# Optimization experiments

Measured on AMD Instinct MI355X. Metric: run time of the kernel, lower is better.

## Reference

```python
import jax, jax.numpy as jnp
import numpy as np

B, N, D = 8, 256, 3          # batch, particles, spatial dims
H = 64                        # hidden_nf (channels)
L = 4                         # num_layers
ENC = 3                       # atom_type, aa_type, aa_pos
IN_NF = ENC + 1               # + time
COORDS_RANGE = 15.0 / L       # tanh=True -> coords_range/n_layers
E = B * N * N                 # fully-connected edges per batch graph


def _linear(key, fin, fout):
    k1, k2 = jax.random.split(key)
    s = 1.0 / np.sqrt(fin)
    w = jax.random.uniform(k1, (fout, fin), minval=-s, maxval=s, dtype=jnp.float32)
    b = jax.random.uniform(k2, (fout,), minval=-s, maxval=s, dtype=jnp.float32)
    return w, b


def setup_inputs() -> dict:
    key = jax.random.key(0)
    ks = jax.random.split(key, 64)
    inp = {
        "t": jax.random.uniform(ks[0], (B, 1), dtype=jnp.float32),
        "x": jax.random.normal(ks[1], (B, N * D), dtype=jnp.float32),
        "atom_type": jax.random.uniform(ks[2], (B, N), dtype=jnp.float32),
        "aa_type": jax.random.uniform(ks[3], (B, N), dtype=jnp.float32),
        "aa_pos": jax.random.uniform(ks[4], (B, N), dtype=jnp.float32),
        "node_mask": jnp.ones((B, N), dtype=jnp.float32),
    }
    inp["emb_w"], inp["emb_b"] = _linear(ks[5], IN_NF, H)
    specs = [("edge_w1", "edge_b1", 2 * H + 2, H), ("edge_w2", "edge_b2", H, H),
             ("node_w1", "node_b1", 2 * H, H), ("node_w2", "node_b2", H, H),
             ("coord_w1", "coord_b1", H, H), ("att_w", "att_b", H, 1)]
    kk = 6
    for wn, bn, fin, fout in specs:
        ws, bs = [], []
        for _ in range(L):
            w, b = _linear(ks[kk], fin, fout); kk += 1
            ws.append(w); bs.append(b)
        inp[wn] = jnp.stack(ws); inp[bn] = jnp.stack(bs)
    # final coord layer: Linear(H,1,bias=False), xavier gain 0.001
    inp["coord_w2"] = jax.random.normal(ks[kk], (L, 1, H), dtype=jnp.float32) * 0.001
    return inp


def _edges():
    idx = jnp.arange(N)
    row_in = jnp.repeat(idx, N)
    col_in = jnp.tile(idx, N)
    off = (jnp.arange(B) * N)[:, None]
    row = (off + row_in[None, :]).reshape(-1)
    col = (off + col_in[None, :]).reshape(-1)
    return row, col


def reference(t, x, atom_type, aa_type, aa_pos, node_mask,
              emb_w, emb_b, edge_w1, edge_b1, edge_w2, edge_b2,
              node_w1, node_b1, node_w2, node_b2,
              coord_w1, coord_b1, att_w, att_b, coord_w2):
    silu = jax.nn.silu
    row, col = _edges()
    nm = node_mask.reshape(B * N, 1)
    # edge mask: pairwise node mask with diagonal (self-loop) removed
    em = ((node_mask[:, :, None] * node_mask[:, None, :])
          * (1.0 - jnp.eye(N, dtype=jnp.float32))).reshape(E, 1)

    x0 = x.reshape(B * N, D) * nm
    tt = jnp.broadcast_to(t, (B, N)).reshape(B * N, 1) * nm
    h = jnp.stack([atom_type, aa_type, aa_pos], axis=-1).reshape(B * N, ENC) * nm
    h = jnp.concatenate([h, tt], axis=1)                      # [BN, 4]
    edge_attr0 = jnp.sum((x0[row] - x0[col]) ** 2, axis=1, keepdims=True)  # [E,1]

    h = h @ emb_w.T + emb_b                                   # embedding -> [BN, H]
    coord = x0
    for l in range(L):
        diff = coord[row] - coord[col]                        # [E, D]
        radial = jnp.sum(diff ** 2, axis=1, keepdims=True)    # [E, 1]
        diff = diff / (jnp.sqrt(radial + 1e-8) + 1.0)         # norm_diff
        m = jnp.concatenate([h[row], h[col], radial, edge_attr0], axis=1)
        m = silu(m @ edge_w1[l].T + edge_b1[l])
        m = silu(m @ edge_w2[l].T + edge_b2[l])               # [E, H]
        m = m * jax.nn.sigmoid(m @ att_w[l].T + att_b[l]) * em
        phi = jnp.tanh(silu(m @ coord_w1[l].T + coord_b1[l]) @ coord_w2[l].T)
        trans = diff * phi * COORDS_RANGE * em                # [E, D]
        coord = (coord + jax.ops.segment_sum(trans, row, num_segments=B * N)) * nm
        agg = jax.ops.segment_sum(m, row, num_segments=B * N)  # [BN, H]
        upd = jnp.concatenate([h, agg], axis=1)
        upd = silu(upd @ node_w1[l].T + node_b1[l]) @ node_w2[l].T + node_b2[l]
        h = (h + upd) * nm                                    # recurrent residual

    vel = (coord - x0) * nm
    vel = vel.reshape(B, N, D)
    nmr = node_mask.reshape(B, N, 1)
    Ns = jnp.sum(nmr, axis=1, keepdims=True)
    vel = vel - (jnp.sum(vel, axis=1, keepdims=True) / Ns) * nmr  # remove_mean_with_mask
    return vel.reshape(B, N * D)
```

## Files before the change

kernel.cpp:

```cpp
#include <hip/hip_runtime.h>

#define CRANGE 3.75f

typedef _Float16 half_t;
typedef __attribute__((ext_vector_type(8))) _Float16 half8;
typedef __attribute__((ext_vector_type(4))) _Float16 half4;
typedef __attribute__((ext_vector_type(4))) float f32x4;

__device__ __forceinline__ float frcp(float x) { return __builtin_amdgcn_rcpf(x); }
__device__ __forceinline__ float fsilu(float x) { return x * frcp(1.f + __expf(-x)); }
__device__ __forceinline__ float fsigm(float x) { return frcp(1.f + __expf(-x)); }
__device__ __forceinline__ float ftanh_(float x) { float e = __expf(2.f * x); return 1.f - 2.f * frcp(e + 1.f); }

__global__ void k_init(const float* __restrict__ t, const float* __restrict__ x,
                       const float* __restrict__ at, const float* __restrict__ aa,
                       const float* __restrict__ ap, const float* __restrict__ nm,
                       const float* __restrict__ embw, const float* __restrict__ embb,
                       float* __restrict__ h, float* __restrict__ x0, float* __restrict__ cA) {
    int idx = blockIdx.x * 256 + threadIdx.x;
    int n = idx >> 6, c = idx & 63;
    float m = nm[n];
    int b = n >> 8;
    float i0 = at[n] * m, i1 = aa[n] * m, i2 = ap[n] * m, i3 = t[b] * m;
    const float* w = embw + c * 4;
    h[idx] = w[0] * i0 + w[1] * i1 + w[2] * i2 + w[3] * i3 + embb[c];
    if (idx < 2048 * 3) {
        int nn = idx / 3;
        float v = x[idx] * nm[nn];
        x0[idx] = v; cA[idx] = v;
    }
}

__global__ void k_prep(const float* __restrict__ ew2, const float* __restrict__ cw1,
                       half_t* __restrict__ wf) {
    int idx = blockIdx.x * 256 + threadIdx.x;
    int lane = idx & 63;
    int g = (idx >> 6) & 7;
    int mat = (idx >> 9) & 1;
    int l = idx >> 10;
    int mt = g >> 1, kc = g & 1;
    int c = lane & 15, qq = lane >> 4;
    const float* W = (mat ? cw1 : ew2) + l * 4096;
    int row = 16 * mt + c;
    int k0 = 32 * kc + 8 * qq;
    half8 pk;
#pragma unroll
    for (int j = 0; j < 8; ++j) pk[j] = (half_t)W[row * 64 + k0 + j];
    ((half8*)wf)[idx] = pk;
}

__global__ void k_nodepre(const float* __restrict__ h, const float* __restrict__ ew1,
                          const float* __restrict__ eb1,
                          float* __restrict__ Hr, float* __restrict__ Hc) {
    int n = blockIdx.x;
    int t = threadIdx.x;
    __shared__ float sh[64];
    if (t < 64) sh[t] = h[n * 64 + t];
    __syncthreads();
    int c = t & 63;
    const float* w = ew1 + c * 130 + ((t >= 64) ? 64 : 0);
    float acc = (t < 64) ? eb1[c] : 0.f;
#pragma unroll
    for (int k = 0; k < 64; ++k) acc += w[k] * sh[k];
    if (t < 64) Hr[n * 64 + c] = acc;
    else        Hc[n * 64 + c] = acc;
}

__global__ __launch_bounds__(256, 3) void k_edge(
    const float* __restrict__ coordIn, const float* __restrict__ x0,
    const float* __restrict__ Hr, const float* __restrict__ Hc,
    const float* __restrict__ ew1, const float* __restrict__ eb2,
    const float* __restrict__ cb1, const float* __restrict__ attw,
    const float* __restrict__ attb, const float* __restrict__ cw2,
    const float* __restrict__ nm, const half_t* __restrict__ wf2,
    const half_t* __restrict__ wf1,
    float* __restrict__ coordOut, float* __restrict__ aggO)
{
    __shared__ __align__(16) half_t sV[4][4096];
    __shared__ __align__(16) float sGeo[4][64][4];
    __shared__ float sHr[64], sWr[64], sWe[64], sB2[64], sBc1[64], sAttw[64], sWc2[64];
    __shared__ float sAgg[64];
    __shared__ float sCoord[3];

    const int i = blockIdx.x, b = i >> 8, ir = i & 255;
    const int t = threadIdx.x, wv = t >> 6, e = t & 63;
    const int q = e >> 4, c = e & 15;
    const int col = (b << 8) + t;

    if (t < 64) {
        sHr[t] = Hr[i * 64 + t];
        sWr[t] = ew1[t * 130 + 128];
        sWe[t] = ew1[t * 130 + 129];
        sB2[t] = eb2[t]; sBc1[t] = cb1[t]; sAttw[t] = attw[t]; sWc2[t] = cw2[t];
        sAgg[t] = 0.f;
    }
    if (t == 64) { sCoord[0] = 0.f; sCoord[1] = 0.f; sCoord[2] = 0.f; }
    float attb0 = attb[0];
    float nmi = nm[i];

    float cix = coordIn[i*3+0], ciy = coordIn[i*3+1], ciz = coordIn[i*3+2];
    float dx = cix - coordIn[col*3+0];
    float dy = ciy - coordIn[col*3+1];
    float dz = ciz - coordIn[col*3+2];
    float radial = dx*dx + dy*dy + dz*dz;
    float inv = frcp(__builtin_amdgcn_sqrtf(radial + 1e-8f) + 1.f);
    float ex = x0[i*3+0] - x0[col*3+0];
    float ey = x0[i*3+1] - x0[col*3+1];
    float ez = x0[i*3+2] - x0[col*3+2];
    float e0 = ex*ex + ey*ey + ez*ez;
    float em = nmi * nm[col] * ((t == ir) ? 0.f : 1.f);

    __syncthreads();

    {
        float4 g4 = make_float4(dx*inv, dy*inv, dz*inv, em);
        *(float4*)&sGeo[wv][e][0] = g4;
    }

    half_t* mybuf = (half_t*)sV[wv];
    const float4* hcv = (const float4*)(Hc + col * 64);
#pragma unroll
    for (int s = 0; s < 8; ++s) {
        float4 ha = hcv[2*s], hb = hcv[2*s+1];
        float v[8];
        v[0]=ha.x; v[1]=ha.y; v[2]=ha.z; v[3]=ha.w;
        v[4]=hb.x; v[5]=hb.y; v[6]=hb.z; v[7]=hb.w;
        half8 pk;
#pragma unroll
        for (int u = 0; u < 8; ++u) {
            int k = 8*s + u;
            pk[u] = (half_t)fsilu(sHr[k] + v[u] + radial * sWr[k] + e0 * sWe[k]);
        }
        int f = (e >> 4) * 2 + (s >> 2);
        *(half8*)&mybuf[f * 512 + ((s & 3) * 16 + c) * 8] = pk;
    }

    const half8* bv = (const half8*)mybuf;
    f32x4 acc[4][4];
#pragma unroll
    for (int mt = 0; mt < 4; ++mt)
#pragma unroll
        for (int nt = 0; nt < 4; ++nt)
#pragma unroll
            for (int r = 0; r < 4; ++r) acc[mt][nt][r] = 0.f;
    {
        const half8* a2v = (const half8*)wf2;
        half8 a2[8];
#pragma unroll
        for (int g = 0; g < 8; ++g) a2[g] = a2v[g * 64 + e];
#pragma unroll
        for (int nt = 0; nt < 4; ++nt) {
            half8 b0 = bv[(nt*2+0)*64 + e];
            half8 b1 = bv[(nt*2+1)*64 + e];
#pragma unroll
            for (int mt = 0; mt < 4; ++mt) {
                acc[mt][nt] = __builtin_amdgcn_mfma_f32_16x16x32_f16(a2[mt*2+0], b0, acc[mt][nt], 0, 0, 0);
                acc[mt][nt] = __builtin_amdgcn_mfma_f32_16x16x32_f16(a2[mt*2+1], b1, acc[mt][nt], 0, 0, 0);
            }
        }
    }

    half8 a1[8];
    {
        const half8* a1v = (const half8*)wf1;
#pragma unroll
        for (int g = 0; g < 8; ++g) a1[g] = a1v[g * 64 + e];
    }

    float attp[4] = {0.f, 0.f, 0.f, 0.f};
#pragma unroll
    for (int mt = 0; mt < 4; ++mt) {
#pragma unroll
        for (int r = 0; r < 4; ++r) {
            int row = 16*mt + 4*q + r;
            float bb = sB2[row], aw = sAttw[row];
#pragma unroll
            for (int nt = 0; nt < 4; ++nt) {
                float v = fsilu(acc[mt][nt][r] + bb);
                acc[mt][nt][r] = v;
                attp[nt] += v * aw;
            }
        }
    }
#pragma unroll
    for (int nt = 0; nt < 4; ++nt) {
        float v = attp[nt];
        v += __shfl_xor(v, 16);
        v += __shfl_xor(v, 32);
        attp[nt] = v;
    }
    float scale[4];
#pragma unroll
    for (int nt = 0; nt < 4; ++nt)
        scale[nt] = fsigm(attp[nt] + attb0) * sGeo[wv][16*nt + c][3];

    float aggp[4][4];
#pragma unroll
    for (int mt = 0; mt < 4; ++mt)
#pragma unroll
        for (int r = 0; r < 4; ++r) aggp[mt][r] = 0.f;
#pragma unroll
    for (int mt = 0; mt < 4; ++mt) {
        int kbase = 16*mt + 4*q;
        int fof = ((kbase >> 5) * 512) + (((kbase >> 3) & 3) * 128) + (kbase & 7);
#pragma unroll
        for (int nt = 0; nt < 4; ++nt) {
            half4 pk;
#pragma unroll
            for (int r = 0; r < 4; ++r) {
                float v = acc[mt][nt][r] * scale[nt];
                aggp[mt][r] += v;
                pk[r] = (half_t)v;
            }
            *(half4*)&mybuf[nt*1024 + fof + c*8] = pk;
        }
    }

#pragma unroll
    for (int mt = 0; mt < 4; ++mt)
#pragma unroll
        for (int r = 0; r < 4; ++r) {
            float v = aggp[mt][r];
            v += __shfl_xor(v, 1); v += __shfl_xor(v, 2);
            v += __shfl_xor(v, 4); v += __shfl_xor(v, 8);
            if (c == 0) atomicAdd(&sAgg[16*mt + 4*q + r], v);
        }

    f32x4 acc2[4][4];
#pragma unroll
    for (int mt = 0; mt < 4; ++mt)
#pragma unroll
        for (int nt = 0; nt < 4; ++nt)
#pragma unroll
            for (int r = 0; r < 4; ++r) acc2[mt][nt][r] = 0.f;
#pragma unroll
    for (int nt = 0; nt < 4; ++nt) {
        half8 b0 = bv[(nt*2+0)*64 + e];
        half8 b1 = bv[(nt*2+1)*64 + e];
#pragma unroll
        for (int mt = 0; mt < 4; ++mt) {
            acc2[mt][nt] = __builtin_amdgcn_mfma_f32_16x16x32_f16(a1[mt*2+0], b0, acc2[mt][nt], 0, 0, 0);
            acc2[mt][nt] = __builtin_amdgcn_mfma_f32_16x16x32_f16(a1[mt*2+1], b1, acc2[mt][nt], 0, 0, 0);
        }
    }

    float php[4] = {0.f, 0.f, 0.f, 0.f};
#pragma unroll
    for (int mt = 0; mt < 4; ++mt) {
#pragma unroll
        for (int r = 0; r < 4; ++r) {
            int row = 16*mt + 4*q + r;
            float bb = sBc1[row], wc = sWc2[row];
#pragma unroll
            for (int nt = 0; nt < 4; ++nt)
                php[nt] += fsilu(acc2[mt][nt][r] + bb) * wc;
        }
    }
#pragma unroll
    for (int nt = 0; nt < 4; ++nt) {
        float v = php[nt];
        v += __shfl_xor(v, 16);
        v += __shfl_xor(v, 32);
        php[nt] = v;
    }
    float tx = 0.f, ty = 0.f, tz = 0.f;
#pragma unroll
    for (int nt = 0; nt < 4; ++nt) {
        int ee = 16*nt + c;
        float4 g4 = *(float4*)&sGeo[wv][ee][0];
        float tr = ftanh_(php[nt]) * CRANGE * g4.w;
        tx += g4.x * tr; ty += g4.y * tr; tz += g4.z * tr;
    }
    tx += __shfl_xor(tx, 1); tx += __shfl_xor(tx, 2); tx += __shfl_xor(tx, 4); tx += __shfl_xor(tx, 8);
    ty += __shfl_xor(ty, 1); ty += __shfl_xor(ty, 2); ty += __shfl_xor(ty, 4); ty += __shfl_xor(ty, 8);
    tz += __shfl_xor(tz, 1); tz += __shfl_xor(tz, 2); tz += __shfl_xor(tz, 4); tz += __shfl_xor(tz, 8);
    if (e == 0) {
        atomicAdd(&sCoord[0], tx);
        atomicAdd(&sCoord[1], ty);
        atomicAdd(&sCoord[2], tz);
    }

    __syncthreads();
    if (t < 64) aggO[i * 64 + t] = sAgg[t];
    if (t >= 64 && t < 67) {
        int d = t - 64;
        coordOut[i * 3 + d] = (coordIn[i * 3 + d] + sCoord[d]) * nmi;
    }
}

__global__ void k_node(const float* __restrict__ nw1, const float* __restrict__ nb1,
                       const float* __restrict__ nw2, const float* __restrict__ nb2,
                       const float* __restrict__ agg, const float* __restrict__ nm,
                       float* __restrict__ h) {
    int n = blockIdx.x;
    int c = threadIdx.x;
    __shared__ float sh[64], sa[64], su[64];
    sh[c] = h[n * 64 + c];
    sa[c] = agg[n * 64 + c];
    __syncthreads();
    const float* w = nw1 + c * 128;
    float acc = nb1[c];
#pragma unroll
    for (int k = 0; k < 64; ++k) acc += w[k] * sh[k];
#pragma unroll
    for (int k = 0; k < 64; ++k) acc += w[64 + k] * sa[k];
    su[c] = fsilu(acc);
    __syncthreads();
    const float* w2 = nw2 + c * 64;
    float acc2 = nb2[c];
#pragma unroll
    for (int k = 0; k < 64; ++k) acc2 += w2[k] * su[k];
    h[n * 64 + c] = (sh[c] + acc2) * nm[n];
}

__global__ void k_final(const float* __restrict__ coord, const float* __restrict__ x0,
                        const float* __restrict__ nm, float* __restrict__ out) {
    int b = blockIdx.x;
    int t = threadIdx.x;
    int i = b * 256 + t;
    int lane = t & 63;
    float m = nm[i];
    float vx = (coord[i * 3 + 0] - x0[i * 3 + 0]) * m;
    float vy = (coord[i * 3 + 1] - x0[i * 3 + 1]) * m;
    float vz = (coord[i * 3 + 2] - x0[i * 3 + 2]) * m;
    __shared__ float red[4];
    if (t < 4) red[t] = 0.f;
    __syncthreads();
    float sx = vx, sy = vy, sz = vz, sn = m;
#pragma unroll
    for (int off = 1; off < 64; off <<= 1) {
        sx += __shfl_xor(sx, off);
        sy += __shfl_xor(sy, off);
        sz += __shfl_xor(sz, off);
        sn += __shfl_xor(sn, off);
    }
    if (lane == 0) {
        atomicAdd(&red[0], sx); atomicAdd(&red[1], sy);
        atomicAdd(&red[2], sz); atomicAdd(&red[3], sn);
    }
    __syncthreads();
    float invNs = frcp(red[3]);
    out[b * 768 + t * 3 + 0] = vx - red[0] * invNs * m;
    out[b * 768 + t * 3 + 1] = vy - red[1] * invNs * m;
    out[b * 768 + t * 3 + 2] = vz - red[2] * invNs * m;
}

extern "C" void kernel_launch(void* const* d_in, const int* in_sizes, int n_in,
                              void* d_out, int out_size, void* d_ws, size_t ws_size,
                              hipStream_t stream) {
    const float* t_in    = (const float*)d_in[0];
    const float* x_in    = (const float*)d_in[1];
    const float* at_in   = (const float*)d_in[2];
    const float* aa_in   = (const float*)d_in[3];
    const float* ap_in   = (const float*)d_in[4];
    const float* nm_in   = (const float*)d_in[5];
    const float* emb_w   = (const float*)d_in[6];
    const float* emb_b   = (const float*)d_in[7];
    const float* edge_w1 = (const float*)d_in[8];
    const float* edge_b1 = (const float*)d_in[9];
    const float* edge_w2 = (const float*)d_in[10];
    const float* edge_b2 = (const float*)d_in[11];
    const float* node_w1 = (const float*)d_in[12];
    const float* node_b1 = (const float*)d_in[13];
    const float* node_w2 = (const float*)d_in[14];
    const float* node_b2 = (const float*)d_in[15];
    const float* coord_w1= (const float*)d_in[16];
    const float* coord_b1= (const float*)d_in[17];
    const float* att_w   = (const float*)d_in[18];
    const float* att_b   = (const float*)d_in[19];
    const float* coord_w2= (const float*)d_in[20];

    float* ws  = (float*)d_ws;
    float* h   = ws;
    float* Hr  = h + 131072;
    float* Hc  = Hr + 131072;
    float* agg = Hc + 131072;
    float* x0  = agg + 131072;
    float* cA  = x0 + 6144;
    float* cB  = cA + 6144;
    half_t* wf = (half_t*)(cB + 6144);

    float* out = (float*)d_out;

    k_prep<<<16, 256, 0, stream>>>(edge_w2, coord_w1, wf);
    k_init<<<512, 256, 0, stream>>>(t_in, x_in, at_in, aa_in, ap_in, nm_in, emb_w, emb_b,
                                    h, x0, cA);

    for (int l = 0; l < 4; ++l) {
        const float* ew1 = edge_w1 + l * 64 * 130;
        const float* eb1 = edge_b1 + l * 64;
        const float* eb2 = edge_b2 + l * 64;
        const float* nw1 = node_w1 + l * 64 * 128;
        const float* nb1 = node_b1 + l * 64;
        const float* nw2 = node_w2 + l * 4096;
        const float* nb2 = node_b2 + l * 64;
        const float* cb1 = coord_b1 + l * 64;
        const float* aw  = att_w + l * 64;
        const float* ab  = att_b + l;
        const float* cw2 = coord_w2 + l * 64;

        const float* cin  = (l & 1) ? cB : cA;
        float*       cout = (l & 1) ? cA : cB;

        k_nodepre<<<2048, 128, 0, stream>>>(h, ew1, eb1, Hr, Hc);
        k_edge<<<2048, 256, 0, stream>>>(cin, x0, Hr, Hc, ew1, eb2, cb1,
                                         aw, ab, cw2, nm_in,
                                         wf + l * 8192, wf + l * 8192 + 4096,
                                         cout, agg);
        k_node<<<2048, 64, 0, stream>>>(nw1, nb1, nw2, nb2, agg, nm_in, h);
    }

    k_final<<<8, 256, 0, stream>>>(cA, x0, nm_in, out);
}
```

Baseline: 344.6 us.

## Fuse node update and next-layer edge precompute into edge kernel, batch reciprocals

Folds the per-node MLP update and the next layer's Hr/Hc projections into the tail of the edge kernel, so the separate k_nodepre and k_node launches go away and the agg buffer is never written to global memory. Hc is double-buffered so the next layer's values can be written while other blocks still read the current ones. Weights are pre-transposed for coalesced access, and the layer-0 projection moves into k_init. The SiLU, sigmoid and tanh reciprocals are batched four at a time into one rcp, exp inputs are clamped, and launch bounds rise to 4 blocks per SM. The node-update tail adds serial synchronisation steps to every edge block.

```diff
diff --git a/kernel.cpp b/kernel.cpp
--- a/kernel.cpp
+++ b/kernel.cpp
@@ -8,73 +8,96 @@
 typedef __attribute__((ext_vector_type(4))) float f32x4;
 
 __device__ __forceinline__ float frcp(float x) { return __builtin_amdgcn_rcpf(x); }
-__device__ __forceinline__ float fsilu(float x) { return x * frcp(1.f + __expf(-x)); }
-__device__ __forceinline__ float fsigm(float x) { return frcp(1.f + __expf(-x)); }
-__device__ __forceinline__ float ftanh_(float x) { float e = __expf(2.f * x); return 1.f - 2.f * frcp(e + 1.f); }
+__device__ __forceinline__ float fexpn(float x) { return __expf(fminf(x, 20.f)); }
+__device__ __forceinline__ float fsilu(float x) { return x * frcp(1.f + fexpn(-x)); }
+
+__device__ __forceinline__ void inv4(float d0, float d1, float d2, float d3, float* o) {
+    float p01 = d0 * d1, p23 = d2 * d3;
+    float r = frcp(p01 * p23);
+    float t01 = p23 * r, t23 = p01 * r;
+    o[0] = d1 * t01; o[1] = d0 * t01; o[2] = d3 * t23; o[3] = d2 * t23;
+}
+__device__ __forceinline__ void silu4(const float* x, float* o) {
+    float d0 = 1.f + fexpn(-x[0]), d1 = 1.f + fexpn(-x[1]);
+    float d2 = 1.f + fexpn(-x[2]), d3 = 1.f + fexpn(-x[3]);
+    float iv[4]; inv4(d0, d1, d2, d3, iv);
+    o[0] = x[0] * iv[0]; o[1] = x[1] * iv[1]; o[2] = x[2] * iv[2]; o[3] = x[3] * iv[3];
+}
+
+__global__ void k_prep(const float* __restrict__ ew2, const float* __restrict__ cw1,
+                       const float* __restrict__ nw1, const float* __restrict__ nw2,
+                       const float* __restrict__ ew1,
+                       half_t* __restrict__ wf, float* __restrict__ trT) {
+    int idx = blockIdx.x * 256 + threadIdx.x;
+    if (idx < 4096) {
+        int lane = idx & 63;
+        int g = (idx >> 6) & 7;
+        int mat = (idx >> 9) & 1;
+        int l = idx >> 10;
+        int mt = g >> 1, kc = g & 1;
+        int c = lane & 15, qq = lane >> 4;
+        const float* W = (mat ? cw1 : ew2) + l * 4096;
+        int row = 16 * mt + c;
+        int k0 = 32 * kc + 8 * qq;
+        half8 pk;
+#pragma unroll
+        for (int j = 0; j < 8; ++j) pk[j] = (half_t)W[row * 64 + k0 + j];
+        ((half8*)wf)[idx] = pk;
+    }
+    int tid2 = idx - 4096;
+    if (tid2 >= 0 && tid2 < 81920) {
+        int l = tid2 / 20480, r = tid2 % 20480;
+        float v;
+        if (r < 8192)       { int k = r >> 6,        c = r & 63; v = nw1[l * 8192 + c * 128 + k]; }
+        else if (r < 12288) { int r2 = r - 8192,  k = r2 >> 6, c = r2 & 63; v = nw2[l * 4096 + c * 64 + k]; }
+        else if (r < 16384) { int r2 = r - 12288, k = r2 >> 6, c = r2 & 63; v = ew1[l * 8320 + c * 130 + k]; }
+        else                { int r2 = r - 16384, k = r2 >> 6, c = r2 & 63; v = ew1[l * 8320 + c * 130 + 64 + k]; }
+        trT[l * 20480 + r] = v;
+    }
+}
 
 __global__ void k_init(const float* __restrict__ t, const float* __restrict__ x,
                        const float* __restrict__ at, const float* __restrict__ aa,
                        const float* __restrict__ ap, const float* __restrict__ nm,
                        const float* __restrict__ embw, const float* __restrict__ embb,
-                       float* __restrict__ h, float* __restrict__ x0, float* __restrict__ cA) {
-    int idx = blockIdx.x * 256 + threadIdx.x;
-    int n = idx >> 6, c = idx & 63;
-    float m = nm[n];
-    int b = n >> 8;
+                       const float* __restrict__ ew1aT0, const float* __restrict__ ew1bT0,
+                       const float* __restrict__ eb1_0,
+                       float* __restrict__ h, float* __restrict__ Hr, float* __restrict__ HcA,
+                       float* __restrict__ x0, float* __restrict__ cA) {
+    int n = blockIdx.x, c = threadIdx.x;
+    __shared__ float sh[64];
+    float m = nm[n]; int b = n >> 8;
     float i0 = at[n] * m, i1 = aa[n] * m, i2 = ap[n] * m, i3 = t[b] * m;
-    const float* w = embw + c * 4;
-    h[idx] = w[0] * i0 + w[1] * i1 + w[2] * i2 + w[3] * i3 + embb[c];
-    if (idx < 2048 * 3) {
-        int nn = idx / 3;
-        float v = x[idx] * nm[nn];
-        x0[idx] = v; cA[idx] = v;
-    }
-}
-
-__global__ void k_prep(const float* __restrict__ ew2, const float* __restrict__ cw1,
-                       half_t* __restrict__ wf) {
-    int idx = blockIdx.x * 256 + threadIdx.x;
-    int lane = idx & 63;
-    int g = (idx >> 6) & 7;
-    int mat = (idx >> 9) & 1;
-    int l = idx >> 10;
-    int mt = g >> 1, kc = g & 1;
-    int c = lane & 15, qq = lane >> 4;
-    const float* W = (mat ? cw1 : ew2) + l * 4096;
-    int row = 16 * mt + c;
-    int k0 = 32 * kc + 8 * qq;
-    half8 pk;
-#pragma unroll
-    for (int j = 0; j < 8; ++j) pk[j] = (half_t)W[row * 64 + k0 + j];
-    ((half8*)wf)[idx] = pk;
-}
-
-__global__ void k_nodepre(const float* __restrict__ h, const float* __restrict__ ew1,
-                          const float* __restrict__ eb1,
-                          float* __restrict__ Hr, float* __restrict__ Hc) {
-    int n = blockIdx.x;
-    int t = threadIdx.x;
-    __shared__ float sh[64];
-    if (t < 64) sh[t] = h[n * 64 + t];
-    __syncthreads();
-    int c = t & 63;
-    const float* w = ew1 + c * 130 + ((t >= 64) ? 64 : 0);
-    float acc = (t < 64) ? eb1[c] : 0.f;
-#pragma unroll
-    for (int k = 0; k < 64; ++k) acc += w[k] * sh[k];
-    if (t < 64) Hr[n * 64 + c] = acc;
-    else        Hc[n * 64 + c] = acc;
-}
-
-__global__ __launch_bounds__(256, 3) void k_edge(
+    float4 w = ((const float4*)embw)[c];
+    float hv = w.x * i0 + w.y * i1 + w.z * i2 + w.w * i3 + embb[c];
+    sh[c] = hv; h[n * 64 + c] = hv;
+    if (c < 3) { float v = x[n * 3 + c] * m; x0[n * 3 + c] = v; cA[n * 3 + c] = v; }
+    __syncthreads();
+    float a = eb1_0[c], bb = 0.f;
+#pragma unroll
+    for (int k = 0; k < 64; ++k) {
+        float hk = sh[k];
+        a  += ew1aT0[k * 64 + c] * hk;
+        bb += ew1bT0[k * 64 + c] * hk;
+    }
+    Hr[n * 64 + c] = a;
+    HcA[n * 64 + c] = bb;
+}
+
+__global__ __launch_bounds__(256, 4) void k_edge(
     const float* __restrict__ coordIn, const float* __restrict__ x0,
-    const float* __restrict__ Hr, const float* __restrict__ Hc,
+    float* __restrict__ Hr, const float* __restrict__ Hc,
     const float* __restrict__ ew1, const float* __restrict__ eb2,
     const float* __restrict__ cb1, const float* __restrict__ attw,
     const float* __restrict__ attb, const float* __restrict__ cw2,
     const float* __restrict__ nm, const half_t* __restrict__ wf2,
     const half_t* __restrict__ wf1,
-    float* __restrict__ coordOut, float* __restrict__ aggO)
+    float* __restrict__ hbuf,
+    const float* __restrict__ nw1T, const float* __restrict__ nw2T,
+    const float* __restrict__ nb1, const float* __restrict__ nb2,
+    const float* __restrict__ ew1aTn, const float* __restrict__ ew1bTn,
+    const float* __restrict__ eb1n,
+    float* __restrict__ HcO, float* __restrict__ coordOut)
 {
     __shared__ __align__(16) half_t sV[4][4096];
     __shared__ __align__(16) float sGeo[4][64][4];
@@ -98,10 +121,9 @@
     float attb0 = attb[0];
     float nmi = nm[i];
 
-    float cix = coordIn[i*3+0], ciy = coordIn[i*3+1], ciz = coordIn[i*3+2];
-    float dx = cix - coordIn[col*3+0];
-    float dy = ciy - coordIn[col*3+1];
-    float dz = ciz - coordIn[col*3+2];
+    float dx = coordIn[i*3+0] - coordIn[col*3+0];
+    float dy = coordIn[i*3+1] - coordIn[col*3+1];
+    float dz = coordIn[i*3+2] - coordIn[col*3+2];
     float radial = dx*dx + dy*dy + dz*dz;
     float inv = frcp(__builtin_amdgcn_sqrtf(radial + 1e-8f) + 1.f);
     float ex = x0[i*3+0] - x0[col*3+0];
@@ -122,16 +144,19 @@
 #pragma unroll
     for (int s = 0; s < 8; ++s) {
         float4 ha = hcv[2*s], hb = hcv[2*s+1];
-        float v[8];
-        v[0]=ha.x; v[1]=ha.y; v[2]=ha.z; v[3]=ha.w;
-        v[4]=hb.x; v[5]=hb.y; v[6]=hb.z; v[7]=hb.w;
-        half8 pk;
+        float z[8], so[8];
+        z[0]=ha.x; z[1]=ha.y; z[2]=ha.z; z[3]=ha.w;
+        z[4]=hb.x; z[5]=hb.y; z[6]=hb.z; z[7]=hb.w;
 #pragma unroll
         for (int u = 0; u < 8; ++u) {
             int k = 8*s + u;
-            pk[u] = (half_t)fsilu(sHr[k] + v[u] + radial * sWr[k] + e0 * sWe[k]);
-        }
-        int f = (e >> 4) * 2 + (s >> 2);
+            z[u] = sHr[k] + z[u] + radial * sWr[k] + e0 * sWe[k];
+        }
+        silu4(z, so); silu4(z + 4, so + 4);
+        half8 pk;
+#pragma unroll
+        for (int u = 0; u < 8; ++u) pk[u] = (half_t)so[u];
+        int f = q * 2 + (s >> 2);
         *(half8*)&mybuf[f * 512 + ((s & 3) * 16 + c) * 8] = pk;
     }
 
@@ -170,15 +195,17 @@
     float attp[4] = {0.f, 0.f, 0.f, 0.f};
 #pragma unroll
     for (int mt = 0; mt < 4; ++mt) {
-#pragma unroll
-        for (int r = 0; r < 4; ++r) {
-            int row = 16*mt + 4*q + r;
-            float bb = sB2[row], aw = sAttw[row];
-#pragma unroll
-            for (int nt = 0; nt < 4; ++nt) {
-                float v = fsilu(acc[mt][nt][r] + bb);
-                acc[mt][nt][r] = v;
-                attp[nt] += v * aw;
+        int row0 = 16*mt + 4*q;
+#pragma unroll
+        for (int nt = 0; nt < 4; ++nt) {
+            float z[4], so[4];
+#pragma unroll
+            for (int r = 0; r < 4; ++r) z[r] = acc[mt][nt][r] + sB2[row0 + r];
+            silu4(z, so);
+#pragma unroll
+            for (int r = 0; r < 4; ++r) {
+                acc[mt][nt][r] = so[r];
+                attp[nt] += so[r] * sAttw[row0 + r];
             }
         }
     }
@@ -190,9 +217,15 @@
         attp[nt] = v;
     }
     float scale[4];
-#pragma unroll
-    for (int nt = 0; nt < 4; ++nt)
-        scale[nt] = fsigm(attp[nt] + attb0) * sGeo[wv][16*nt + c][3];
+    {
+        float d0 = 1.f + fexpn(-(attp[0] + attb0));
+        float d1 = 1.f + fexpn(-(attp[1] + attb0));
+        float d2 = 1.f + fexpn(-(attp[2] + attb0));
+        float d3 = 1.f + fexpn(-(attp[3] + attb0));
+        float iv[4]; inv4(d0, d1, d2, d3, iv);
+#pragma unroll
+        for (int nt = 0; nt < 4; ++nt) scale[nt] = iv[nt] * sGeo[wv][16*nt + c][3];
+    }
 
     float aggp[4][4];
 #pragma unroll
@@ -247,13 +280,15 @@
     float php[4] = {0.f, 0.f, 0.f, 0.f};
 #pragma unroll
     for (int mt = 0; mt < 4; ++mt) {
-#pragma unroll
-        for (int r = 0; r < 4; ++r) {
-            int row = 16*mt + 4*q + r;
-            float bb = sBc1[row], wc = sWc2[row];
-#pragma unroll
-            for (int nt = 0; nt < 4; ++nt)
-                php[nt] += fsilu(acc2[mt][nt][r] + bb) * wc;
+        int row0 = 16*mt + 4*q;
+#pragma unroll
+        for (int nt = 0; nt < 4; ++nt) {
+            float z[4], so[4];
+#pragma unroll
+            for (int r = 0; r < 4; ++r) z[r] = acc2[mt][nt][r] + sBc1[row0 + r];
+            silu4(z, so);
+#pragma unroll
+            for (int r = 0; r < 4; ++r) php[nt] += so[r] * sWc2[row0 + r];
         }
     }
 #pragma unroll
@@ -263,12 +298,21 @@
         v += __shfl_xor(v, 32);
         php[nt] = v;
     }
+    float tnh[4];
+    {
+        float d0 = fexpn(2.f * php[0]) + 1.f;
+        float d1 = fexpn(2.f * php[1]) + 1.f;
+        float d2 = fexpn(2.f * php[2]) + 1.f;
+        float d3 = fexpn(2.f * php[3]) + 1.f;
+        float iv[4]; inv4(d0, d1, d2, d3, iv);
+#pragma unroll
+        for (int nt = 0; nt < 4; ++nt) tnh[nt] = 1.f - 2.f * iv[nt];
+    }
     float tx = 0.f, ty = 0.f, tz = 0.f;
 #pragma unroll
     for (int nt = 0; nt < 4; ++nt) {
-        int ee = 16*nt + c;
-        float4 g4 = *(float4*)&sGeo[wv][ee][0];
-        float tr = ftanh_(php[nt]) * CRANGE * g4.w;
+        float4 g4 = *(float4*)&sGeo[wv][16*nt + c][0];
+        float tr = tnh[nt] * CRANGE * g4.w;
         tx += g4.x * tr; ty += g4.y * tr; tz += g4.z * tr;
     }
     tx += __shfl_xor(tx, 1); tx += __shfl_xor(tx, 2); tx += __shfl_xor(tx, 4); tx += __shfl_xor(tx, 8);
@@ -281,36 +325,65 @@
     }
 
     __syncthreads();
-    if (t < 64) aggO[i * 64 + t] = sAgg[t];
-    if (t >= 64 && t < 67) {
-        int d = t - 64;
+
+    float* sT   = (float*)&sV[0][0];
+    float* sIn  = sT;
+    float* sP   = sT + 128;
+    float* sU   = sT + 384;
+    float* sHn  = sT + 448;
+    float* sPB  = sT + 512;
+
+    if (t < 64) sIn[t] = hbuf[i * 64 + t];
+    else if (t < 128) sIn[t] = sAgg[t - 64];
+    if (t >= 128 && t < 131) {
+        int d = t - 128;
         coordOut[i * 3 + d] = (coordIn[i * 3 + d] + sCoord[d]) * nmi;
     }
-}
-
-__global__ void k_node(const float* __restrict__ nw1, const float* __restrict__ nb1,
-                       const float* __restrict__ nw2, const float* __restrict__ nb2,
-                       const float* __restrict__ agg, const float* __restrict__ nm,
-                       float* __restrict__ h) {
-    int n = blockIdx.x;
-    int c = threadIdx.x;
-    __shared__ float sh[64], sa[64], su[64];
-    sh[c] = h[n * 64 + c];
-    sa[c] = agg[n * 64 + c];
-    __syncthreads();
-    const float* w = nw1 + c * 128;
-    float acc = nb1[c];
-#pragma unroll
-    for (int k = 0; k < 64; ++k) acc += w[k] * sh[k];
-#pragma unroll
-    for (int k = 0; k < 64; ++k) acc += w[64 + k] * sa[k];
-    su[c] = fsilu(acc);
-    __syncthreads();
-    const float* w2 = nw2 + c * 64;
-    float acc2 = nb2[c];
-#pragma unroll
-    for (int k = 0; k < 64; ++k) acc2 += w2[k] * su[k];
-    h[n * 64 + c] = (sh[c] + acc2) * nm[n];
+    __syncthreads();
+
+    const int cc = t & 63, p = t >> 6;
+    {
+        float a = 0.f;
+        const float* w = nw1T + (p * 32) * 64 + cc;
+#pragma unroll
+        for (int k = 0; k < 32; ++k) a += w[k * 64] * sIn[p * 32 + k];
+        sP[p * 64 + cc] = a;
+    }
+    __syncthreads();
+    if (t < 64) sU[t] = fsilu(sP[t] + sP[64 + t] + sP[128 + t] + sP[192 + t] + nb1[t]);
+    __syncthreads();
+    {
+        float a = 0.f;
+        const float* w = nw2T + (p * 16) * 64 + cc;
+#pragma unroll
+        for (int k = 0; k < 16; ++k) a += w[k * 64] * sU[p * 16 + k];
+        sP[p * 64 + cc] = a;
+    }
+    __syncthreads();
+    if (t < 64) {
+        float hn = (sIn[t] + sP[t] + sP[64 + t] + sP[128 + t] + sP[192 + t] + nb2[t]) * nmi;
+        hbuf[i * 64 + t] = hn;
+        sHn[t] = hn;
+    }
+    __syncthreads();
+    {
+        float a = 0.f, b2 = 0.f;
+        const float* wa = ew1aTn + (p * 16) * 64 + cc;
+        const float* wb = ew1bTn + (p * 16) * 64 + cc;
+#pragma unroll
+        for (int k = 0; k < 16; ++k) {
+            float hv = sHn[p * 16 + k];
+            a  += wa[k * 64] * hv;
+            b2 += wb[k * 64] * hv;
+        }
+        sP[p * 64 + cc] = a;
+        sPB[p * 64 + cc] = b2;
+    }
+    __syncthreads();
+    if (t < 64) {
+        Hr[i * 64 + t]  = sP[t] + sP[64 + t] + sP[128 + t] + sP[192 + t] + eb1n[t];
+        HcO[i * 64 + t] = sPB[t] + sPB[64 + t] + sPB[128 + t] + sPB[192 + t];
+    }
 }
 
 __global__ void k_final(const float* __restrict__ coord, const float* __restrict__ x0,
@@ -373,41 +446,47 @@
     float* ws  = (float*)d_ws;
     float* h   = ws;
     float* Hr  = h + 131072;
-    float* Hc  = Hr + 131072;
-    float* agg = Hc + 131072;
-    float* x0  = agg + 131072;
+    float* HcA = Hr + 131072;
+    float* HcB = HcA + 131072;
+    float* x0  = HcB + 131072;
     float* cA  = x0 + 6144;
     float* cB  = cA + 6144;
-    half_t* wf = (half_t*)(cB + 6144);
+    float* base = cB + 6144;
+    half_t* wf = (half_t*)base;
+    float* trT = base + 16384;
 
     float* out = (float*)d_out;
 
-    k_prep<<<16, 256, 0, stream>>>(edge_w2, coord_w1, wf);
-    k_init<<<512, 256, 0, stream>>>(t_in, x_in, at_in, aa_in, ap_in, nm_in, emb_w, emb_b,
-                                    h, x0, cA);
+    k_prep<<<336, 256, 0, stream>>>(edge_w2, coord_w1, node_w1, node_w2, edge_w1, wf, trT);
+    k_init<<<2048, 64, 0, stream>>>(t_in, x_in, at_in, aa_in, ap_in, nm_in, emb_w, emb_b,
+                                    trT + 12288, trT + 16384, edge_b1,
+                                    h, Hr, HcA, x0, cA);
 
     for (int l = 0; l < 4; ++l) {
-        const float* ew1 = edge_w1 + l * 64 * 130;
-        const float* eb1 = edge_b1 + l * 64;
+        const float* ew1 = edge_w1 + l * 8320;
         const float* eb2 = edge_b2 + l * 64;
-        const float* nw1 = node_w1 + l * 64 * 128;
-        const float* nb1 = node_b1 + l * 64;
-        const float* nw2 = node_w2 + l * 4096;
-        const float* nb2 = node_b2 + l * 64;
         const float* cb1 = coord_b1 + l * 64;
         const float* aw  = att_w + l * 64;
         const float* ab  = att_b + l;
         const float* cw2 = coord_w2 + l * 64;
+        const float* nb1 = node_b1 + l * 64;
+        const float* nb2 = node_b2 + l * 64;
+
+        const float* trL = trT + l * 20480;
+        int ln = (l + 1) & 3;
+        const float* trN = trT + ln * 20480;
 
         const float* cin  = (l & 1) ? cB : cA;
         float*       cout = (l & 1) ? cA : cB;
-
-        k_nodepre<<<2048, 128, 0, stream>>>(h, ew1, eb1, Hr, Hc);
-        k_edge<<<2048, 256, 0, stream>>>(cin, x0, Hr, Hc, ew1, eb2, cb1,
+        const float* HcR  = (l & 1) ? HcB : HcA;
+        float*       HcW  = (l & 1) ? HcA : HcB;
+
+        k_edge<<<2048, 256, 0, stream>>>(cin, x0, Hr, HcR, ew1, eb2, cb1,
                                          aw, ab, cw2, nm_in,
                                          wf + l * 8192, wf + l * 8192 + 4096,
-                                         cout, agg);
-        k_node<<<2048, 64, 0, stream>>>(nw1, nb1, nw2, nb2, agg, nm_in, h);
+                                         h, trL, trL + 8192, nb1, nb2,
+                                         trN + 12288, trN + 16384, edge_b1 + ln * 64,
+                                         HcW, cout);
     }
 
     k_final<<<8, 256, 0, stream>>>(cA, x0, nm_in, out);
```

Measured after the change: 308.7 us. -10.4%, faster.
